# Optimization experiments

Hardware: AMD Instinct MI355X
Metric: run time of the kernel (lower is better)

The kernel has to match this reference:

```python
import jax, jax.numpy as jnp
import numpy as np

DIM = 256
HEADS = 8
PS = 8  # patch/window size
EPS = 1e-5


def _ln(x, g, b):
    m = x.mean(-1, keepdims=True)
    v = x.var(-1, keepdims=True)
    return (x - m) / jnp.sqrt(v + EPS) * g + b


def setup_inputs() -> dict:
    key = jax.random.key(0)
    ks = jax.random.split(key, 10)
    B, C, H, W = 4, DIM, 256, 256
    s = 0.02
    return {
        "y_lf": jax.random.normal(ks[0], (B, C, H, W), jnp.float32),
        "y_hf": jax.random.normal(ks[1], (B, C, H, W), jnp.float32),
        "g_lf": jnp.ones((C,), jnp.float32),
        "b_lf": jnp.zeros((C,), jnp.float32),
        "g_hf": jnp.ones((C,), jnp.float32),
        "b_hf": jnp.zeros((C,), jnp.float32),
        "Wq": jax.random.normal(ks[2], (C, C), jnp.float32) * s,
        "bq": jnp.zeros((C,), jnp.float32),
        "Wk": jax.random.normal(ks[3], (C, C), jnp.float32) * s,
        "bk": jnp.zeros((C,), jnp.float32),
        "Wv": jax.random.normal(ks[4], (C, C), jnp.float32) * s,
        "bv": jnp.zeros((C,), jnp.float32),
        "Wo": jax.random.normal(ks[5], (C, C), jnp.float32) * s,
        "bo": jnp.zeros((C,), jnp.float32),
    }


def reference(y_lf, y_hf, g_lf, b_lf, g_hf, b_hf, Wq, bq, Wk, bk, Wv, bv, Wo, bo):
    B, C, H, W = y_lf.shape
    ps = PS
    hd = C // HEADS
    nH, nW = H // ps, W // ps

    def win_tokens(x):
        # (B,C,H,W) -> (B*nH*nW, ps*ps, C)
        x = x.reshape(B, C, nH, ps, nW, ps)
        return x.transpose(0, 2, 4, 3, 5, 1).reshape(-1, ps * ps, C)

    lf = win_tokens(y_lf)
    hf = win_tokens(y_hf)  # residual + V source (un-normalized, as in torch code)

    q = _ln(lf, g_lf, b_lf) @ Wq.T + bq
    k = _ln(hf, g_hf, b_hf) @ Wk.T + bk
    v = hf @ Wv.T + bv

    BW, L, _ = q.shape
    q = q.reshape(BW, L, HEADS, hd)
    k = k.reshape(BW, L, HEADS, hd)
    v = v.reshape(BW, L, HEADS, hd)

    scale = 1.0 / np.sqrt(hd).astype(np.float32)
    scores = jnp.einsum('bqhd,bkhd->bhqk', q, k) * scale
    attn = jax.nn.softmax(scores, axis=-1)
    o = jnp.einsum('bhqk,bkhd->bqhd', attn, v).reshape(BW, L, C)
    o = o @ Wo.T + bo + hf  # out_proj + residual

    # window_reverse: (B*nH*nW, ps*ps, C) -> (B,C,H,W)
    o = o.reshape(B, nH, nW, ps, ps, C)
    o = o.transpose(0, 5, 1, 3, 2, 4).reshape(B, C, H, W)
    return o
```

## Files before the change

kernel.cpp:

```cpp
#include <hip/hip_runtime.h>

typedef float  f4     __attribute__((ext_vector_type(4)));
typedef float  f32x4  __attribute__((ext_vector_type(4)));
typedef short  short8 __attribute__((ext_vector_type(8)));
typedef __bf16 bf16x8 __attribute__((ext_vector_type(8)));
typedef int    int4v  __attribute__((ext_vector_type(4)));
typedef unsigned short us4 __attribute__((ext_vector_type(4)));

__device__ __forceinline__ unsigned short f2bf(float f) {
    unsigned int u = __builtin_bit_cast(unsigned int, f);
    u += 0x7FFFu + ((u >> 16) & 1u);
    return (unsigned short)(u >> 16);
}
__device__ __forceinline__ float bf2f(unsigned short h) {
    unsigned int u = ((unsigned int)h) << 16;
    return __builtin_bit_cast(float, u);
}
__device__ __forceinline__ f32x4 mfma_bf16(short8 a, short8 b, f32x4 c) {
    return __builtin_amdgcn_mfma_f32_16x16x32_bf16(
        __builtin_bit_cast(bf16x8, a), __builtin_bit_cast(bf16x8, b), c, 0, 0, 0);
}
__device__ __forceinline__ int cvt_pk_bf16(float lo, float hi) {
    int d;
    asm volatile("v_cvt_pk_bf16_f32 %0, %1, %2" : "=v"(d) : "v"(lo), "v"(hi));
    return d;
}
__device__ __forceinline__ int bperm(int addr, int src) {
    return __builtin_amdgcn_ds_bpermute(addr, src);
}

__global__ void pcaf_precvt(const float* __restrict__ Wq, const float* __restrict__ bq,
                            const float* __restrict__ Wk, const float* __restrict__ bk,
                            const float* __restrict__ Wv, const float* __restrict__ Wo,
                            const float* __restrict__ g_lf, const float* __restrict__ b_lf,
                            const float* __restrict__ g_hf, const float* __restrict__ b_hf,
                            void* __restrict__ ws) {
    const int mat  = blockIdx.x >> 8;
    const int row  = blockIdx.x & 255;
    const int lane = threadIdx.x;
    const float* W = (mat == 0) ? Wq : (mat == 1) ? Wk : (mat == 2) ? Wv : Wo;
    f4 w = *(const f4*)(W + row * 256 + lane * 4);
    f4 wp = w;
    if (mat < 2) {
        const float* g = mat ? g_hf : g_lf;
        f4 gg = *(const f4*)(g + lane * 4);
        wp = w * gg;
    }
    us4 u;
    u[0] = f2bf(wp[0]); u[1] = f2bf(wp[1]); u[2] = f2bf(wp[2]); u[3] = f2bf(wp[3]);
    {
        const int ct   = row >> 4;
        const int l15r = row & 15;
        const int k_   = lane >> 3;
        const int g_   = (lane >> 1) & 3;
        const int e4   = (lane & 1) * 4;
        unsigned short* dst = (unsigned short*)ws + mat * 65536 +
                              (((ct * 8 + k_) * 64) + g_ * 16 + l15r) * 8 + e4;
        *(us4*)dst = u;
    }
    if (mat < 2) {
        const float* b = mat ? b_hf : b_lf;
        f4 bb = *(const f4*)(b + lane * 4);
        float rsum = wp[0] + wp[1] + wp[2] + wp[3];
        float cb   = bb[0] * w[0] + bb[1] * w[1] + bb[2] * w[2] + bb[3] * w[3];
        #pragma unroll
        for (int d = 1; d < 64; d <<= 1) {
            rsum += __shfl_xor(rsum, d);
            cb   += __shfl_xor(cb, d);
        }
        if (lane == 0) {
            float* cons = (float*)((char*)ws + 524288);
            cons[mat * 512 + row]       = rsum;
            cons[mat * 512 + 256 + row] = cb + (mat ? bk[row] : bq[row]);
        }
    }
}

constexpr int RS = 528;

struct AccW { f32x4 a[4][2]; };

__device__ __forceinline__ AccW gemmW(const char* base,
                                      const unsigned short* __restrict__ Wbw,
                                      int lane, int g, int l15) {
    AccW r;
    f32x4 z = {0.f, 0.f, 0.f, 0.f};
    #pragma unroll
    for (int m = 0; m < 4; ++m) { r.a[m][0] = z; r.a[m][1] = z; }
    #pragma unroll
    for (int half = 0; half < 2; ++half) {
        short8 w0[4], w1[4];
        #pragma unroll
        for (int k = 0; k < 4; ++k) {
            w0[k] = *(const short8*)(Wbw + (half * 4 + k) * 512 + lane * 8);
            w1[k] = *(const short8*)(Wbw + 4096 + (half * 4 + k) * 512 + lane * 8);
        }
        #pragma unroll
        for (int k = 0; k < 4; ++k) {
            #pragma unroll
            for (int m = 0; m < 4; ++m) {
                short8 am = *(const short8*)(base + (16 * m + l15) * RS +
                                             ((half * 4 + k) * 32 + g * 8) * 2);
                r.a[m][0] = mfma_bf16(am, w0[k], r.a[m][0]);
                r.a[m][1] = mfma_bf16(am, w1[k], r.a[m][1]);
            }
        }
    }
    return r;
}

__global__ __attribute__((amdgpu_flat_work_group_size(1024, 1024)))
void pcaf6_kernel(
    const float* __restrict__ y_lf, const float* __restrict__ y_hf,
    const float* __restrict__ bv, const float* __restrict__ bo,
    const void* __restrict__ ws, float* __restrict__ out)
{
    constexpr int C = 256, H = 256, W = 256, HW = H * W;
    constexpr int OA = 0;
    constexpr int OB = 67584;
    constexpr int OS = 135168;
    __shared__ __align__(16) char sm[137216];

    const unsigned short* wsq = (const unsigned short*)ws;
    const unsigned short* wsk = wsq + 65536;
    const unsigned short* wsv = wsq + 131072;
    const unsigned short* wso = wsq + 196608;
    const float* cons = (const float*)((const char*)ws + 524288);

    const int tid = threadIdx.x;
    const int bid = blockIdx.x;
    const int wi  = ((bid & 7) << 8) | (bid >> 3);
    const int bb  = wi >> 9;
    const int nh  = (wi >> 4) & 31;
    const int nwp = wi & 15;
    const long pair_base = (long)bb * C * HW + (long)(nh * 8) * W + nwp * 16;

    const int wave = tid >> 6;
    const int win  = wave >> 3;
    const int head = wave & 7;
    const int lane = tid & 63;
    const int g    = lane >> 4;
    const int l15  = lane & 15;
    const int c0   = 32 * head + l15;
    const int ro   = win * 64;

    {
        f4 lv[8], hv[8];
        #pragma unroll
        for (int it = 0; it < 4; ++it) {
            int q2  = it * 1024 + tid;
            int c2  = q2 >> 5;
            int ph  = (q2 >> 2) & 7;
            int pw4 = (q2 & 3) * 4;
            long go = pair_base + (long)(2 * c2) * HW + ph * W + pw4;
            lv[2 * it]     = *(const f4*)(y_lf + go);
            lv[2 * it + 1] = *(const f4*)(y_lf + go + HW);
            hv[2 * it]     = *(const f4*)(y_hf + go);
            hv[2 * it + 1] = *(const f4*)(y_hf + go + HW);
        }
        #pragma unroll
        for (int it = 0; it < 4; ++it) {
            int q2  = it * 1024 + tid;
            int c2  = q2 >> 5;
            int ph  = (q2 >> 2) & 7;
            int pw4 = (q2 & 3) * 4;
            int tok0 = (pw4 >> 3) * 64 + ph * 8 + (pw4 & 7);
            #pragma unroll
            for (int j = 0; j < 4; ++j) {
                unsigned int lvv = (unsigned int)f2bf(lv[2 * it][j]) | ((unsigned int)f2bf(lv[2 * it + 1][j]) << 16);
                unsigned int hvv = (unsigned int)f2bf(hv[2 * it][j]) | ((unsigned int)f2bf(hv[2 * it + 1][j]) << 16);
                *(unsigned int*)(sm + OA + (tok0 + j) * RS + c2 * 4) = lvv;
                *(unsigned int*)(sm + OB + (tok0 + j) * RS + c2 * 4) = hvv;
            }
        }
    }
    __syncthreads();

    {
        const int t = tid >> 3, j = tid & 7;
        #pragma unroll
        for (int pass = 0; pass < 2; ++pass) {
            const int base = pass ? OB : OA;
            float sum = 0.f, ss = 0.f;
            #pragma unroll
            for (int r = 0; r < 4; ++r) {
                short8 raw = *(const short8*)(sm + base + t * RS + (j * 32 + r * 8) * 2);
                #pragma unroll
                for (int e = 0; e < 8; ++e) { float f = bf2f((unsigned short)raw[e]); sum += f; ss += f * f; }
            }
            sum += __shfl_xor(sum, 1); ss += __shfl_xor(ss, 1);
            sum += __shfl_xor(sum, 2); ss += __shfl_xor(ss, 2);
            sum += __shfl_xor(sum, 4); ss += __shfl_xor(ss, 4);
            float mean = sum * (1.f / 256.f);
            float rstd = rsqrtf(ss * (1.f / 256.f) - mean * mean + 1e-5f);
            if (j == 0) {
                float* S = (float*)(sm + OS);
                S[pass * 256 + t]       = mean;
                S[pass * 256 + 128 + t] = rstd;
            }
        }
    }

    AccW qacc = gemmW(sm + OA + ro * RS, wsq + head * 8192, lane, g, l15);

    unsigned int resp[4][2][2];
    #pragma unroll
    for (int m = 0; m < 4; ++m)
        #pragma unroll
        for (int n = 0; n < 2; ++n)
            #pragma unroll
            for (int jh = 0; jh < 2; ++jh) {
                unsigned int lo = *(const unsigned short*)(sm + OB + (ro + 16 * m + 4 * g + 2 * jh) * RS + (c0 + 16 * n) * 2);
                unsigned int hi = *(const unsigned short*)(sm + OB + (ro + 16 * m + 4 * g + 2 * jh + 1) * RS + (c0 + 16 * n) * 2);
                resp[m][n][jh] = lo | (hi << 16);
            }

    int vp[4][2][2];
    {
        AccW vacc = gemmW(sm + OB + ro * RS, wsv + head * 8192, lane, g, l15);
        float bv0 = bv[c0], bv1 = bv[c0 + 16];
        #pragma unroll
        for (int m = 0; m < 4; ++m) {
            vp[m][0][0] = cvt_pk_bf16(vacc.a[m][0][0] + bv0, vacc.a[m][0][1] + bv0);
            vp[m][0][1] = cvt_pk_bf16(vacc.a[m][0][2] + bv0, vacc.a[m][0][3] + bv0);
            vp[m][1][0] = cvt_pk_bf16(vacc.a[m][1][0] + bv1, vacc.a[m][1][1] + bv1);
            vp[m][1][1] = cvt_pk_bf16(vacc.a[m][1][2] + bv1, vacc.a[m][1][3] + bv1);
        }
    }
    __syncthreads();

    {
        const float* S = (const float*)(sm + OS);
        const float SCALE = 0.17677669529663687f;
        float rs0 = cons[c0], rs1 = cons[c0 + 16];
        float cb0 = cons[256 + c0], cb1 = cons[256 + c0 + 16];
        #pragma unroll
        for (int m = 0; m < 4; ++m)
            #pragma unroll
            for (int i = 0; i < 4; ++i) {
                int t = ro + 16 * m + 4 * g + i;
                float mean = S[t], rstd = S[128 + t];
                float v0 = (rstd * (qacc.a[m][0][i] - mean * rs0) + cb0) * SCALE;
                float v1 = (rstd * (qacc.a[m][1][i] - mean * rs1) + cb1) * SCALE;
                *(unsigned short*)(sm + OA + t * RS + c0 * 2)        = f2bf(v0);
                *(unsigned short*)(sm + OA + t * RS + (c0 + 16) * 2) = f2bf(v1);
            }
    }

    AccW kacc = gemmW(sm + OB + ro * RS, wsk + head * 8192, lane, g, l15);
    __syncthreads();

    {
        const float* S = (const float*)(sm + OS);
        float rs0 = cons[512 + c0], rs1 = cons[512 + c0 + 16];
        float cb0 = cons[768 + c0], cb1 = cons[768 + c0 + 16];
        #pragma unroll
        for (int m = 0; m < 4; ++m)
            #pragma unroll
            for (int i = 0; i < 4; ++i) {
                int t = ro + 16 * m + 4 * g + i;
                float mean = S[256 + t], rstd = S[384 + t];
                float v0 = rstd * (kacc.a[m][0][i] - mean * rs0) + cb0;
                float v1 = rstd * (kacc.a[m][1][i] - mean * rs1) + cb1;
                *(unsigned short*)(sm + OB + t * RS + c0 * 2)        = f2bf(v0);
                *(unsigned short*)(sm + OB + t * RS + (c0 + 16) * 2) = f2bf(v1);
            }
    }
    __syncthreads();

    {
        short8 kf[4], qf[4];
        #pragma unroll
        for (int x = 0; x < 4; ++x) {
            kf[x] = *(const short8*)(sm + OB + (ro + 16 * x + l15) * RS + (32 * head + 8 * g) * 2);
            qf[x] = *(const short8*)(sm + OA + (ro + 16 * x + l15) * RS + (32 * head + 8 * g) * 2);
        }
        __syncthreads();

        f32x4 z = {0.f, 0.f, 0.f, 0.f};

        const int a0 = ((2 * (g & 1)) * 16 + l15) * 4;
        const int a1 = a0 + 64;
        const bool ghi = (g >> 1) & 1;

        short8 vf[2][2];
        #pragma unroll
        for (int kk = 0; kk < 2; ++kk)
            #pragma unroll
            for (int n2 = 0; n2 < 2; ++n2) {
                int4v t;
                #pragma unroll
                for (int j = 0; j < 4; ++j) {
                    int ad = (j >> 1) ? a1 : a0;
                    int v0 = bperm(ad, vp[2 * kk][n2][j & 1]);
                    int v1 = bperm(ad, vp[2 * kk + 1][n2][j & 1]);
                    t[j] = ghi ? v1 : v0;
                }
                vf[kk][n2] = __builtin_bit_cast(short8, t);
            }

        f32x4 o[4][2];
        #pragma unroll
        for (int c = 0; c < 4; ++c) { o[c][0] = z; o[c][1] = z; }

        #pragma unroll
        for (int c = 0; c < 4; ++c) {
            f32x4 stc[4];
            #pragma unroll
            for (int nk = 0; nk < 4; ++nk)
                stc[nk] = mfma_bf16(kf[nk], qf[c], z);

            float mx = stc[0][0];
            #pragma unroll
            for (int nk = 0; nk < 4; ++nk)
                #pragma unroll
                for (int i = 0; i < 4; ++i) mx = fmaxf(mx, stc[nk][i]);
            mx = fmaxf(mx, __shfl_xor(mx, 16));
            mx = fmaxf(mx, __shfl_xor(mx, 32));
            float sum = 0.f;
            #pragma unroll
            for (int nk = 0; nk < 4; ++nk)
                #pragma unroll
                for (int i = 0; i < 4; ++i) {
                    float e = __expf(stc[nk][i] - mx);
                    stc[nk][i] = e;
                    sum += e;
                }
            sum += __shfl_xor(sum, 16);
            sum += __shfl_xor(sum, 32);
            float is = 1.f / sum;

            int p[4][2];
            #pragma unroll
            for (int nk = 0; nk < 4; ++nk) {
                p[nk][0] = cvt_pk_bf16(stc[nk][0] * is, stc[nk][1] * is);
                p[nk][1] = cvt_pk_bf16(stc[nk][2] * is, stc[nk][3] * is);
            }

            #pragma unroll
            for (int kk = 0; kk < 2; ++kk) {
                int4v t;
                #pragma unroll
                for (int j = 0; j < 4; ++j) {
                    int ad = (j >> 1) ? a1 : a0;
                    int v0 = bperm(ad, p[2 * kk][j & 1]);
                    int v1 = bperm(ad, p[2 * kk + 1][j & 1]);
                    t[j] = ghi ? v1 : v0;
                }
                short8 pf = __builtin_bit_cast(short8, t);
                o[c][0] = mfma_bf16(pf, vf[kk][0], o[c][0]);
                o[c][1] = mfma_bf16(pf, vf[kk][1], o[c][1]);
            }
        }

        #pragma unroll
        for (int c = 0; c < 4; ++c)
            #pragma unroll
            for (int i = 0; i < 4; ++i) {
                int t = ro + 16 * c + 4 * g + i;
                *(unsigned short*)(sm + OA + t * RS + c0 * 2)        = f2bf(o[c][0][i]);
                *(unsigned short*)(sm + OA + t * RS + (c0 + 16) * 2) = f2bf(o[c][1][i]);
            }
    }
    __syncthreads();

    {
        AccW oacc = gemmW(sm + OA + ro * RS, wso + head * 8192, lane, g, l15);
        const long win_base = pair_base + win * 8;
        float bo0 = bo[c0], bo1 = bo[c0 + 16];
        #pragma unroll
        for (int n = 0; n < 2; ++n) {
            float bon = n ? bo1 : bo0;
            int cout = c0 + 16 * n;
            #pragma unroll
            for (int m = 0; m < 4; ++m) {
                int tok0 = 16 * m + 4 * g;
                int ph = tok0 >> 3, pw = tok0 & 7;
                f4 ov;
                #pragma unroll
                for (int i = 0; i < 4; ++i) {
                    float rv = bf2f((unsigned short)((resp[m][n][i >> 1] >> (16 * (i & 1))) & 0xFFFF));
                    ov[i] = oacc.a[m][n][i] + bon + rv;
                }
                *(f4*)(out + win_base + (long)cout * HW + ph * W + pw) = ov;
            }
        }
    }
}

extern "C" void kernel_launch(void* const* d_in, const int* in_sizes, int n_in,
                              void* d_out, int out_size, void* d_ws, size_t ws_size,
                              hipStream_t stream) {
    (void)in_sizes; (void)n_in; (void)out_size; (void)ws_size;
    const float* y_lf = (const float*)d_in[0];
    const float* y_hf = (const float*)d_in[1];
    const float* g_lf = (const float*)d_in[2];
    const float* b_lf = (const float*)d_in[3];
    const float* g_hf = (const float*)d_in[4];
    const float* b_hf = (const float*)d_in[5];
    const float* Wq   = (const float*)d_in[6];
    const float* bq   = (const float*)d_in[7];
    const float* Wk   = (const float*)d_in[8];
    const float* bk   = (const float*)d_in[9];
    const float* Wv   = (const float*)d_in[10];
    const float* bv   = (const float*)d_in[11];
    const float* Wo   = (const float*)d_in[12];
    const float* bo   = (const float*)d_in[13];
    float* out = (float*)d_out;

    pcaf_precvt<<<dim3(1024), dim3(64), 0, stream>>>(
        Wq, bq, Wk, bk, Wv, Wo, g_lf, b_lf, g_hf, b_hf, d_ws);
    pcaf6_kernel<<<dim3(2048), dim3(1024), 0, stream>>>(
        y_lf, y_hf, bv, bo, d_ws, out);
}
```

Measured before the change: 480.5 us.

## Make fused attention kernel persistent with prefetch of next window pair and staged output stores

The grid shrinks from 2048 to 512 blocks, and each block loops over four window pairs. The global loads for the next pair are issued into registers before the current pair's output epilogue, so load latency overlaps the store phase. Output is now staged through shared memory and written as coalesced 16-wide rows instead of scattered 8-wide per-window stores. The block-to-window swizzle is dropped, a waves_per_eu hint is added, and the extra prefetch registers and syncs may raise register pressure.

```diff
diff --git a/kernel.cpp b/kernel.cpp
--- a/kernel.cpp
+++ b/kernel.cpp
@@ -76,7 +76,12 @@
     }
 }
 
-constexpr int RS = 528;
+constexpr int RS  = 528;
+constexpr int HWC = 65536;
+constexpr int Wd  = 256;
+constexpr int OA  = 0;
+constexpr int OB  = 67584;
+constexpr int OS  = 135168;
 
 struct AccW { f32x4 a[4][2]; };
 
@@ -109,16 +114,29 @@
     return r;
 }
 
-__global__ __attribute__((amdgpu_flat_work_group_size(1024, 1024)))
-void pcaf6_kernel(
+__device__ __forceinline__ void issue_pair_loads(
+    const float* __restrict__ y_lf, const float* __restrict__ y_hf,
+    long pair_base, int tid, f4* lv, f4* hv) {
+    #pragma unroll
+    for (int it = 0; it < 4; ++it) {
+        int q2  = it * 1024 + tid;
+        int c2  = q2 >> 5;
+        int ph  = (q2 >> 2) & 7;
+        int pw4 = (q2 & 3) * 4;
+        long go = pair_base + (long)(2 * c2) * HWC + ph * Wd + pw4;
+        lv[2 * it]     = *(const f4*)(y_lf + go);
+        lv[2 * it + 1] = *(const f4*)(y_lf + go + HWC);
+        hv[2 * it]     = *(const f4*)(y_hf + go);
+        hv[2 * it + 1] = *(const f4*)(y_hf + go + HWC);
+    }
+}
+
+__global__ __attribute__((amdgpu_flat_work_group_size(1024, 1024), amdgpu_waves_per_eu(4, 4)))
+void pcaf7_kernel(
     const float* __restrict__ y_lf, const float* __restrict__ y_hf,
     const float* __restrict__ bv, const float* __restrict__ bo,
     const void* __restrict__ ws, float* __restrict__ out)
 {
-    constexpr int C = 256, H = 256, W = 256, HW = H * W;
-    constexpr int OA = 0;
-    constexpr int OB = 67584;
-    constexpr int OS = 135168;
     __shared__ __align__(16) char sm[137216];
 
     const unsigned short* wsq = (const unsigned short*)ws;
@@ -129,11 +147,6 @@
 
     const int tid = threadIdx.x;
     const int bid = blockIdx.x;
-    const int wi  = ((bid & 7) << 8) | (bid >> 3);
-    const int bb  = wi >> 9;
-    const int nh  = (wi >> 4) & 31;
-    const int nwp = wi & 15;
-    const long pair_base = (long)bb * C * HW + (long)(nh * 8) * W + nwp * 16;
 
     const int wave = tid >> 6;
     const int win  = wave >> 3;
@@ -144,20 +157,16 @@
     const int c0   = 32 * head + l15;
     const int ro   = win * 64;
 
+    f4 lv[8], hv[8];
+    long pair_base;
     {
-        f4 lv[8], hv[8];
-        #pragma unroll
-        for (int it = 0; it < 4; ++it) {
-            int q2  = it * 1024 + tid;
-            int c2  = q2 >> 5;
-            int ph  = (q2 >> 2) & 7;
-            int pw4 = (q2 & 3) * 4;
-            long go = pair_base + (long)(2 * c2) * HW + ph * W + pw4;
-            lv[2 * it]     = *(const f4*)(y_lf + go);
-            lv[2 * it + 1] = *(const f4*)(y_lf + go + HW);
-            hv[2 * it]     = *(const f4*)(y_hf + go);
-            hv[2 * it + 1] = *(const f4*)(y_hf + go + HW);
-        }
+        int pp = bid;
+        int bb = pp >> 9, nh = (pp >> 4) & 31, nwp = pp & 15;
+        pair_base = (long)bb * 256 * HWC + (long)(nh * 8) * Wd + nwp * 16;
+        issue_pair_loads(y_lf, y_hf, pair_base, tid, lv, hv);
+    }
+
+    for (int p = 0; p < 4; ++p) {
         #pragma unroll
         for (int it = 0; it < 4; ++it) {
             int q2  = it * 1024 + tid;
@@ -173,218 +182,241 @@
                 *(unsigned int*)(sm + OB + (tok0 + j) * RS + c2 * 4) = hvv;
             }
         }
-    }
-    __syncthreads();
-
-    {
-        const int t = tid >> 3, j = tid & 7;
-        #pragma unroll
-        for (int pass = 0; pass < 2; ++pass) {
-            const int base = pass ? OB : OA;
-            float sum = 0.f, ss = 0.f;
-            #pragma unroll
-            for (int r = 0; r < 4; ++r) {
-                short8 raw = *(const short8*)(sm + base + t * RS + (j * 32 + r * 8) * 2);
-                #pragma unroll
-                for (int e = 0; e < 8; ++e) { float f = bf2f((unsigned short)raw[e]); sum += f; ss += f * f; }
-            }
-            sum += __shfl_xor(sum, 1); ss += __shfl_xor(ss, 1);
-            sum += __shfl_xor(sum, 2); ss += __shfl_xor(ss, 2);
-            sum += __shfl_xor(sum, 4); ss += __shfl_xor(ss, 4);
-            float mean = sum * (1.f / 256.f);
-            float rstd = rsqrtf(ss * (1.f / 256.f) - mean * mean + 1e-5f);
-            if (j == 0) {
-                float* S = (float*)(sm + OS);
-                S[pass * 256 + t]       = mean;
-                S[pass * 256 + 128 + t] = rstd;
-            }
-        }
-    }
-
-    AccW qacc = gemmW(sm + OA + ro * RS, wsq + head * 8192, lane, g, l15);
-
-    unsigned int resp[4][2][2];
-    #pragma unroll
-    for (int m = 0; m < 4; ++m)
-        #pragma unroll
-        for (int n = 0; n < 2; ++n)
-            #pragma unroll
-            for (int jh = 0; jh < 2; ++jh) {
-                unsigned int lo = *(const unsigned short*)(sm + OB + (ro + 16 * m + 4 * g + 2 * jh) * RS + (c0 + 16 * n) * 2);
-                unsigned int hi = *(const unsigned short*)(sm + OB + (ro + 16 * m + 4 * g + 2 * jh + 1) * RS + (c0 + 16 * n) * 2);
-                resp[m][n][jh] = lo | (hi << 16);
-            }
-
-    int vp[4][2][2];
-    {
-        AccW vacc = gemmW(sm + OB + ro * RS, wsv + head * 8192, lane, g, l15);
-        float bv0 = bv[c0], bv1 = bv[c0 + 16];
-        #pragma unroll
-        for (int m = 0; m < 4; ++m) {
-            vp[m][0][0] = cvt_pk_bf16(vacc.a[m][0][0] + bv0, vacc.a[m][0][1] + bv0);
-            vp[m][0][1] = cvt_pk_bf16(vacc.a[m][0][2] + bv0, vacc.a[m][0][3] + bv0);
-            vp[m][1][0] = cvt_pk_bf16(vacc.a[m][1][0] + bv1, vacc.a[m][1][1] + bv1);
-            vp[m][1][1] = cvt_pk_bf16(vacc.a[m][1][2] + bv1, vacc.a[m][1][3] + bv1);
-        }
-    }
-    __syncthreads();
-
-    {
-        const float* S = (const float*)(sm + OS);
-        const float SCALE = 0.17677669529663687f;
-        float rs0 = cons[c0], rs1 = cons[c0 + 16];
-        float cb0 = cons[256 + c0], cb1 = cons[256 + c0 + 16];
+        const long cur_base = pair_base;
+        __syncthreads();
+
+        {
+            const int t = tid >> 3, j = tid & 7;
+            #pragma unroll
+            for (int pass = 0; pass < 2; ++pass) {
+                const int base = pass ? OB : OA;
+                float sum = 0.f, ss = 0.f;
+                #pragma unroll
+                for (int r = 0; r < 4; ++r) {
+                    short8 raw = *(const short8*)(sm + base + t * RS + (j * 32 + r * 8) * 2);
+                    #pragma unroll
+                    for (int e = 0; e < 8; ++e) { float f = bf2f((unsigned short)raw[e]); sum += f; ss += f * f; }
+                }
+                sum += __shfl_xor(sum, 1); ss += __shfl_xor(ss, 1);
+                sum += __shfl_xor(sum, 2); ss += __shfl_xor(ss, 2);
+                sum += __shfl_xor(sum, 4); ss += __shfl_xor(ss, 4);
+                float mean = sum * (1.f / 256.f);
+                float rstd = rsqrtf(ss * (1.f / 256.f) - mean * mean + 1e-5f);
+                if (j == 0) {
+                    float* S = (float*)(sm + OS);
+                    S[pass * 256 + t]       = mean;
+                    S[pass * 256 + 128 + t] = rstd;
+                }
+            }
+        }
+
+        AccW qacc = gemmW(sm + OA + ro * RS, wsq + head * 8192, lane, g, l15);
+
+        unsigned int resp[4][2][2];
         #pragma unroll
         for (int m = 0; m < 4; ++m)
             #pragma unroll
-            for (int i = 0; i < 4; ++i) {
-                int t = ro + 16 * m + 4 * g + i;
-                float mean = S[t], rstd = S[128 + t];
-                float v0 = (rstd * (qacc.a[m][0][i] - mean * rs0) + cb0) * SCALE;
-                float v1 = (rstd * (qacc.a[m][1][i] - mean * rs1) + cb1) * SCALE;
-                *(unsigned short*)(sm + OA + t * RS + c0 * 2)        = f2bf(v0);
-                *(unsigned short*)(sm + OA + t * RS + (c0 + 16) * 2) = f2bf(v1);
-            }
-    }
-
-    AccW kacc = gemmW(sm + OB + ro * RS, wsk + head * 8192, lane, g, l15);
-    __syncthreads();
-
-    {
-        const float* S = (const float*)(sm + OS);
-        float rs0 = cons[512 + c0], rs1 = cons[512 + c0 + 16];
-        float cb0 = cons[768 + c0], cb1 = cons[768 + c0 + 16];
-        #pragma unroll
-        for (int m = 0; m < 4; ++m)
-            #pragma unroll
-            for (int i = 0; i < 4; ++i) {
-                int t = ro + 16 * m + 4 * g + i;
-                float mean = S[256 + t], rstd = S[384 + t];
-                float v0 = rstd * (kacc.a[m][0][i] - mean * rs0) + cb0;
-                float v1 = rstd * (kacc.a[m][1][i] - mean * rs1) + cb1;
-                *(unsigned short*)(sm + OB + t * RS + c0 * 2)        = f2bf(v0);
-                *(unsigned short*)(sm + OB + t * RS + (c0 + 16) * 2) = f2bf(v1);
-            }
-    }
-    __syncthreads();
-
-    {
-        short8 kf[4], qf[4];
-        #pragma unroll
-        for (int x = 0; x < 4; ++x) {
-            kf[x] = *(const short8*)(sm + OB + (ro + 16 * x + l15) * RS + (32 * head + 8 * g) * 2);
-            qf[x] = *(const short8*)(sm + OA + (ro + 16 * x + l15) * RS + (32 * head + 8 * g) * 2);
-        }
-        __syncthreads();
-
-        f32x4 z = {0.f, 0.f, 0.f, 0.f};
-
-        const int a0 = ((2 * (g & 1)) * 16 + l15) * 4;
-        const int a1 = a0 + 64;
-        const bool ghi = (g >> 1) & 1;
-
-        short8 vf[2][2];
-        #pragma unroll
-        for (int kk = 0; kk < 2; ++kk)
-            #pragma unroll
-            for (int n2 = 0; n2 < 2; ++n2) {
-                int4v t;
-                #pragma unroll
-                for (int j = 0; j < 4; ++j) {
-                    int ad = (j >> 1) ? a1 : a0;
-                    int v0 = bperm(ad, vp[2 * kk][n2][j & 1]);
-                    int v1 = bperm(ad, vp[2 * kk + 1][n2][j & 1]);
-                    t[j] = ghi ? v1 : v0;
-                }
-                vf[kk][n2] = __builtin_bit_cast(short8, t);
-            }
-
-        f32x4 o[4][2];
-        #pragma unroll
-        for (int c = 0; c < 4; ++c) { o[c][0] = z; o[c][1] = z; }
-
-        #pragma unroll
-        for (int c = 0; c < 4; ++c) {
-            f32x4 stc[4];
-            #pragma unroll
-            for (int nk = 0; nk < 4; ++nk)
-                stc[nk] = mfma_bf16(kf[nk], qf[c], z);
-
-            float mx = stc[0][0];
-            #pragma unroll
-            for (int nk = 0; nk < 4; ++nk)
-                #pragma unroll
-                for (int i = 0; i < 4; ++i) mx = fmaxf(mx, stc[nk][i]);
-            mx = fmaxf(mx, __shfl_xor(mx, 16));
-            mx = fmaxf(mx, __shfl_xor(mx, 32));
-            float sum = 0.f;
-            #pragma unroll
-            for (int nk = 0; nk < 4; ++nk)
+            for (int n = 0; n < 2; ++n)
+                #pragma unroll
+                for (int jh = 0; jh < 2; ++jh) {
+                    unsigned int lo = *(const unsigned short*)(sm + OB + (ro + 16 * m + 4 * g + 2 * jh) * RS + (c0 + 16 * n) * 2);
+                    unsigned int hi = *(const unsigned short*)(sm + OB + (ro + 16 * m + 4 * g + 2 * jh + 1) * RS + (c0 + 16 * n) * 2);
+                    resp[m][n][jh] = lo | (hi << 16);
+                }
+
+        int vp[4][2][2];
+        {
+            AccW vacc = gemmW(sm + OB + ro * RS, wsv + head * 8192, lane, g, l15);
+            float bv0 = bv[c0], bv1 = bv[c0 + 16];
+            #pragma unroll
+            for (int m = 0; m < 4; ++m) {
+                vp[m][0][0] = cvt_pk_bf16(vacc.a[m][0][0] + bv0, vacc.a[m][0][1] + bv0);
+                vp[m][0][1] = cvt_pk_bf16(vacc.a[m][0][2] + bv0, vacc.a[m][0][3] + bv0);
+                vp[m][1][0] = cvt_pk_bf16(vacc.a[m][1][0] + bv1, vacc.a[m][1][1] + bv1);
+                vp[m][1][1] = cvt_pk_bf16(vacc.a[m][1][2] + bv1, vacc.a[m][1][3] + bv1);
+            }
+        }
+        __syncthreads();
+
+        {
+            const float* S = (const float*)(sm + OS);
+            const float SCALE = 0.17677669529663687f;
+            float rs0 = cons[c0], rs1 = cons[c0 + 16];
+            float cb0 = cons[256 + c0], cb1 = cons[256 + c0 + 16];
+            #pragma unroll
+            for (int m = 0; m < 4; ++m)
                 #pragma unroll
                 for (int i = 0; i < 4; ++i) {
-                    float e = __expf(stc[nk][i] - mx);
-                    stc[nk][i] = e;
-                    sum += e;
-                }
-            sum += __shfl_xor(sum, 16);
-            sum += __shfl_xor(sum, 32);
-            float is = 1.f / sum;
-
-            int p[4][2];
-            #pragma unroll
-            for (int nk = 0; nk < 4; ++nk) {
-                p[nk][0] = cvt_pk_bf16(stc[nk][0] * is, stc[nk][1] * is);
-                p[nk][1] = cvt_pk_bf16(stc[nk][2] * is, stc[nk][3] * is);
-            }
-
-            #pragma unroll
-            for (int kk = 0; kk < 2; ++kk) {
-                int4v t;
-                #pragma unroll
-                for (int j = 0; j < 4; ++j) {
-                    int ad = (j >> 1) ? a1 : a0;
-                    int v0 = bperm(ad, p[2 * kk][j & 1]);
-                    int v1 = bperm(ad, p[2 * kk + 1][j & 1]);
-                    t[j] = ghi ? v1 : v0;
-                }
-                short8 pf = __builtin_bit_cast(short8, t);
-                o[c][0] = mfma_bf16(pf, vf[kk][0], o[c][0]);
-                o[c][1] = mfma_bf16(pf, vf[kk][1], o[c][1]);
-            }
-        }
-
-        #pragma unroll
-        for (int c = 0; c < 4; ++c)
-            #pragma unroll
-            for (int i = 0; i < 4; ++i) {
-                int t = ro + 16 * c + 4 * g + i;
-                *(unsigned short*)(sm + OA + t * RS + c0 * 2)        = f2bf(o[c][0][i]);
-                *(unsigned short*)(sm + OA + t * RS + (c0 + 16) * 2) = f2bf(o[c][1][i]);
-            }
-    }
-    __syncthreads();
-
-    {
+                    int t = ro + 16 * m + 4 * g + i;
+                    float mean = S[t], rstd = S[128 + t];
+                    float v0 = (rstd * (qacc.a[m][0][i] - mean * rs0) + cb0) * SCALE;
+                    float v1 = (rstd * (qacc.a[m][1][i] - mean * rs1) + cb1) * SCALE;
+                    *(unsigned short*)(sm + OA + t * RS + c0 * 2)        = f2bf(v0);
+                    *(unsigned short*)(sm + OA + t * RS + (c0 + 16) * 2) = f2bf(v1);
+                }
+        }
+
+        AccW kacc = gemmW(sm + OB + ro * RS, wsk + head * 8192, lane, g, l15);
+        __syncthreads();
+
+        {
+            const float* S = (const float*)(sm + OS);
+            float rs0 = cons[512 + c0], rs1 = cons[512 + c0 + 16];
+            float cb0 = cons[768 + c0], cb1 = cons[768 + c0 + 16];
+            #pragma unroll
+            for (int m = 0; m < 4; ++m)
+                #pragma unroll
+                for (int i = 0; i < 4; ++i) {
+                    int t = ro + 16 * m + 4 * g + i;
+                    float mean = S[256 + t], rstd = S[384 + t];
+                    float v0 = rstd * (kacc.a[m][0][i] - mean * rs0) + cb0;
+                    float v1 = rstd * (kacc.a[m][1][i] - mean * rs1) + cb1;
+                    *(unsigned short*)(sm + OB + t * RS + c0 * 2)        = f2bf(v0);
+                    *(unsigned short*)(sm + OB + t * RS + (c0 + 16) * 2) = f2bf(v1);
+                }
+        }
+        __syncthreads();
+
+        {
+            short8 kf[4], qf[4];
+            #pragma unroll
+            for (int x = 0; x < 4; ++x) {
+                kf[x] = *(const short8*)(sm + OB + (ro + 16 * x + l15) * RS + (32 * head + 8 * g) * 2);
+                qf[x] = *(const short8*)(sm + OA + (ro + 16 * x + l15) * RS + (32 * head + 8 * g) * 2);
+            }
+            __syncthreads();
+
+            f32x4 z = {0.f, 0.f, 0.f, 0.f};
+            const int a0 = ((2 * (g & 1)) * 16 + l15) * 4;
+            const int a1 = a0 + 64;
+            const bool ghi = (g >> 1) & 1;
+
+            short8 vf[2][2];
+            #pragma unroll
+            for (int kk = 0; kk < 2; ++kk)
+                #pragma unroll
+                for (int n2 = 0; n2 < 2; ++n2) {
+                    int4v t;
+                    #pragma unroll
+                    for (int j = 0; j < 4; ++j) {
+                        int ad = (j >> 1) ? a1 : a0;
+                        int v0 = bperm(ad, vp[2 * kk][n2][j & 1]);
+                        int v1 = bperm(ad, vp[2 * kk + 1][n2][j & 1]);
+                        t[j] = ghi ? v1 : v0;
+                    }
+                    vf[kk][n2] = __builtin_bit_cast(short8, t);
+                }
+
+            f32x4 o[4][2];
+            #pragma unroll
+            for (int c = 0; c < 4; ++c) { o[c][0] = z; o[c][1] = z; }
+
+            #pragma unroll
+            for (int c = 0; c < 4; ++c) {
+                f32x4 stc[4];
+                #pragma unroll
+                for (int nk = 0; nk < 4; ++nk)
+                    stc[nk] = mfma_bf16(kf[nk], qf[c], z);
+
+                float mx = stc[0][0];
+                #pragma unroll
+                for (int nk = 0; nk < 4; ++nk)
+                    #pragma unroll
+                    for (int i = 0; i < 4; ++i) mx = fmaxf(mx, stc[nk][i]);
+                mx = fmaxf(mx, __shfl_xor(mx, 16));
+                mx = fmaxf(mx, __shfl_xor(mx, 32));
+                float sum = 0.f;
+                #pragma unroll
+                for (int nk = 0; nk < 4; ++nk)
+                    #pragma unroll
+                    for (int i = 0; i < 4; ++i) {
+                        float e = __expf(stc[nk][i] - mx);
+                        stc[nk][i] = e;
+                        sum += e;
+                    }
+                sum += __shfl_xor(sum, 16);
+                sum += __shfl_xor(sum, 32);
+                float is = 1.f / sum;
+
+                int pq[4][2];
+                #pragma unroll
+                for (int nk = 0; nk < 4; ++nk) {
+                    pq[nk][0] = cvt_pk_bf16(stc[nk][0] * is, stc[nk][1] * is);
+                    pq[nk][1] = cvt_pk_bf16(stc[nk][2] * is, stc[nk][3] * is);
+                }
+
+                #pragma unroll
+                for (int kk = 0; kk < 2; ++kk) {
+                    int4v t;
+                    #pragma unroll
+                    for (int j = 0; j < 4; ++j) {
+                        int ad = (j >> 1) ? a1 : a0;
+                        int v0 = bperm(ad, pq[2 * kk][j & 1]);
+                        int v1 = bperm(ad, pq[2 * kk + 1][j & 1]);
+                        t[j] = ghi ? v1 : v0;
+                    }
+                    short8 pf = __builtin_bit_cast(short8, t);
+                    o[c][0] = mfma_bf16(pf, vf[kk][0], o[c][0]);
+                    o[c][1] = mfma_bf16(pf, vf[kk][1], o[c][1]);
+                }
+            }
+
+            #pragma unroll
+            for (int c = 0; c < 4; ++c)
+                #pragma unroll
+                for (int i = 0; i < 4; ++i) {
+                    int t = ro + 16 * c + 4 * g + i;
+                    *(unsigned short*)(sm + OA + t * RS + c0 * 2)        = f2bf(o[c][0][i]);
+                    *(unsigned short*)(sm + OA + t * RS + (c0 + 16) * 2) = f2bf(o[c][1][i]);
+                }
+        }
+        __syncthreads();
+
         AccW oacc = gemmW(sm + OA + ro * RS, wso + head * 8192, lane, g, l15);
-        const long win_base = pair_base + win * 8;
-        float bo0 = bo[c0], bo1 = bo[c0 + 16];
-        #pragma unroll
-        for (int n = 0; n < 2; ++n) {
-            float bon = n ? bo1 : bo0;
-            int cout = c0 + 16 * n;
-            #pragma unroll
-            for (int m = 0; m < 4; ++m) {
-                int tok0 = 16 * m + 4 * g;
-                int ph = tok0 >> 3, pw = tok0 & 7;
-                f4 ov;
-                #pragma unroll
-                for (int i = 0; i < 4; ++i) {
-                    float rv = bf2f((unsigned short)((resp[m][n][i >> 1] >> (16 * (i & 1))) & 0xFFFF));
-                    ov[i] = oacc.a[m][n][i] + bon + rv;
-                }
-                *(f4*)(out + win_base + (long)cout * HW + ph * W + pw) = ov;
-            }
-        }
+        __syncthreads();
+
+        if (p + 1 < 4) {
+            int pp = bid + 512 * (p + 1);
+            int bb = pp >> 9, nh = (pp >> 4) & 31, nwp = pp & 15;
+            pair_base = (long)bb * 256 * HWC + (long)(nh * 8) * Wd + nwp * 16;
+            issue_pair_loads(y_lf, y_hf, pair_base, tid, lv, hv);
+        }
+
+        {
+            float bo0 = bo[c0], bo1 = bo[c0 + 16];
+            #pragma unroll
+            for (int n = 0; n < 2; ++n) {
+                float bon = n ? bo1 : bo0;
+                int cout = c0 + 16 * n;
+                #pragma unroll
+                for (int m = 0; m < 4; ++m) {
+                    int ph  = 2 * m + (g >> 1);
+                    int pw4 = 4 * (g & 1);
+                    f4 ov;
+                    #pragma unroll
+                    for (int i = 0; i < 4; ++i) {
+                        float rv = bf2f((unsigned short)((resp[m][n][i >> 1] >> (16 * (i & 1))) & 0xFFFF));
+                        ov[i] = oacc.a[m][n][i] + bon + rv;
+                    }
+                    *(f4*)(sm + cout * 528 + (ph * 16 + win * 8 + pw4) * 4) = ov;
+                }
+            }
+        }
+        __syncthreads();
+
+        {
+            #pragma unroll
+            for (int it = 0; it < 8; ++it) {
+                int idx = it * 1024 + tid;
+                int c   = idx >> 5;
+                int rem = idx & 31;
+                int ph  = rem >> 2;
+                int l4  = rem & 3;
+                f4 v = *(const f4*)(sm + c * 528 + ph * 64 + l4 * 16);
+                *(f4*)(out + cur_base + (long)c * HWC + ph * Wd + l4 * 4) = v;
+            }
+        }
+        __syncthreads();
     }
 }
 
@@ -410,6 +442,6 @@
 
     pcaf_precvt<<<dim3(1024), dim3(64), 0, stream>>>(
         Wq, bq, Wk, bk, Wv, Wo, g_lf, b_lf, g_hf, b_hf, d_ws);
-    pcaf6_kernel<<<dim3(2048), dim3(1024), 0, stream>>>(
+    pcaf7_kernel<<<dim3(512), dim3(1024), 0, stream>>>(
         y_lf, y_hf, bv, bo, d_ws, out);
 }
```

Result: slower. 1.466 ms (+205.1%).
